# Performance work log

Hardware: AMD Instinct MI355X
Metric: run time of the kernel (lower is better)

Reference implementation:

```python
import jax, jax.numpy as jnp
import numpy as np

N = 16384      # total points
B = 8          # point clouds in batch
PER = N // B   # points per cloud (batch ids sorted in blocks)
M = 4096       # sampled centers (ratio 0.25, strided sampler -> batch-aligned)
K = 64         # max_num_neighbors
R = 0.25       # ball-query radius
C_IN = 128
HID = 256
C_OUT = 256


def setup_inputs() -> dict:
    key = jax.random.key(0)
    k1, k2, k3, k4, k5 = jax.random.split(key, 5)
    x = jax.random.normal(k1, (N, C_IN), dtype=jnp.float32)
    pos = jax.random.uniform(k2, (N, 3), dtype=jnp.float32)  # unit cube
    batch = jnp.repeat(jnp.arange(B, dtype=jnp.int32), PER)  # sorted block batch ids
    lframes = jax.random.normal(k3, (N, 3, 3), dtype=jnp.float32)
    W1 = jax.random.normal(k4, (2 * C_IN + 3, HID), dtype=jnp.float32) * 0.05
    b1 = jnp.zeros((HID,), dtype=jnp.float32)
    W2 = jax.random.normal(k5, (HID, C_OUT), dtype=jnp.float32) * 0.05
    b2 = jnp.zeros((C_OUT,), dtype=jnp.float32)
    return {"x": x, "pos": pos, "batch": batch, "lframes": lframes,
            "W1": W1, "b1": b1, "W2": W2, "b2": b2}


def _ball_query(pos, batch, idx):
    """radius(pos, pos[idx], R, batch, batch[idx], max_num_neighbors=K).
    Returns fixed-size neighbor indices [M, K] + validity mask [M, K]."""
    pos_c = pos[idx]                                  # [M, 3]
    # squared distances via gemm trick (avoid [M, N, 3] broadcast)
    d2 = ((pos_c ** 2).sum(-1)[:, None]
          + (pos ** 2).sum(-1)[None, :]
          - 2.0 * pos_c @ pos.T)                      # [M, N]
    valid = (d2 <= R * R) & (batch[idx][:, None] == batch[None, :])
    score = jnp.where(valid, -d2, -jnp.inf)
    vals, nbr = jax.lax.top_k(score, K)               # K nearest within ball
    return nbr, jnp.isfinite(vals)


def reference(x, pos, batch, lframes, W1, b1, W2, b2):
    # center sampler: strided subsample (batch-aligned since batch is block-sorted)
    idx = jnp.arange(0, N, N // M)                    # [M]
    nbr, vmask = _ball_query(pos, batch, idx)         # [M, K]

    pos_dst = pos[idx]                                # [M, 3]
    x_dst = x[idx]                                    # [M, C_IN]
    lframes_dst = lframes[idx]                        # [M, 3, 3]

    # EdgeConv: per-edge message MLP([x_src, x_dst, lframe_dst @ (pos_src - pos_dst)])
    rel = pos[nbr] - pos_dst[:, None, :]              # [M, K, 3]
    rel_loc = jnp.einsum('mij,mkj->mki', lframes_dst, rel)  # rotate into dst frame
    feats = jnp.concatenate([
        x[nbr],                                        # [M, K, C_IN]
        jnp.broadcast_to(x_dst[:, None, :], (M, K, C_IN)),
        rel_loc,
    ], axis=-1)                                        # [M, K, 2*C_IN+3]

    h = jax.nn.relu(feats @ W1 + b1)                   # [M, K, HID]
    msg = h @ W2 + b2                                  # [M, K, C_OUT]

    # masked max aggregation over valid neighbors
    msg = jnp.where(vmask[..., None], msg, -jnp.inf)
    out = msg.max(axis=1)                              # [M, C_OUT]
    out = jnp.where(jnp.isfinite(out), out, 0.0)
    return out, pos_dst, batch[idx], lframes_dst
```

## Files before the change

kernel.cpp:

```cpp
#include <hip/hip_runtime.h>
#include <hip/hip_bf16.h>

#define N_PTS 16384
#define PER   2048
#define M_CTR 4096
#define KNB   64
#define C_IN  128
#define HID   256
#define C_OUT 256

typedef unsigned short u16;
typedef unsigned int u32;
typedef __attribute__((ext_vector_type(8))) short s8v;
typedef __attribute__((ext_vector_type(4))) float f4v;
typedef __attribute__((ext_vector_type(4))) unsigned int u4v;

static __device__ __forceinline__ u16 f2bf(float f) {
    union { float f; unsigned int i; } v; v.f = f;
    unsigned int r = v.i + 0x7FFFu + ((v.i >> 16) & 1u);
    return (u16)(r >> 16);
}

__global__ __launch_bounds__(256) void ballq_kernel(
        const float* __restrict__ pos, int* __restrict__ nbr, int* __restrict__ cnt,
        const float* __restrict__ W1, const float* __restrict__ W2,
        u16* __restrict__ W1aT, u16* __restrict__ W1bT, u16* __restrict__ W2T) {
    __shared__ float cd2[1024];
    __shared__ int   cidx[1024];
    __shared__ int   s_n;
    int m = blockIdx.x, tid = threadIdx.x;

    if (m < 256) {
        int gid = m * 256 + tid;
        int cc = gid >> 8, k = gid & 255;
        W2T[gid] = f2bf(W2[k * 256 + cc]);
        if (gid < 32768) {
            int c1 = gid >> 7, k1 = gid & 127;
            W1aT[gid] = f2bf(W1[k1 * 256 + c1]);
            W1bT[gid] = f2bf(W1[(k1 + 128) * 256 + c1]);
        }
    }

    int c = m * 4;
    int base = (m >> 9) << 11;
    int ln = tid & 63;
    if (tid == 0) s_n = 0;
    __syncthreads();
    float cx = pos[c * 3 + 0], cy = pos[c * 3 + 1], cz = pos[c * 3 + 2];
    float A = __fadd_rn(__fadd_rn(__fmul_rn(cx, cx), __fmul_rn(cy, cy)), __fmul_rn(cz, cz));
    float c2x = __fmul_rn(2.0f, cx);
    float c2y = __fmul_rn(2.0f, cy);
    float c2z = __fmul_rn(2.0f, cz);
    for (int s = 0; s < 8; ++s) {
        int j = base + tid + (s << 8);
        float px = pos[j * 3 + 0], py = pos[j * 3 + 1], pz = pos[j * 3 + 2];
        float B = __fadd_rn(__fadd_rn(__fmul_rn(px, px), __fmul_rn(py, py)), __fmul_rn(pz, pz));
        float C = __fmaf_rn(c2z, pz, __fmaf_rn(c2y, py, __fmul_rn(c2x, px)));
        float d2 = __fsub_rn(__fadd_rn(A, B), C);
        bool hit = (d2 <= 0.0625f);
        unsigned long long mk = __ballot(hit);
        int nb = __popcll(mk & ((1ull << ln) - 1ull));
        int tot = __popcll(mk);
        int bidx = 0;
        if (ln == 0 && tot) bidx = atomicAdd(&s_n, tot);
        bidx = __shfl(bidx, 0, 64);
        if (hit) {
            int a = bidx + nb;
            if (a < 1024) { cd2[a] = d2; cidx[a] = j; }
        }
    }
    __syncthreads();
    int V = s_n < 1024 ? s_n : 1024;
    if (V <= KNB) {
        if (tid < KNB) nbr[m * KNB + tid] = (tid < V) ? cidx[tid] : c;
        if (tid == 0) cnt[m] = V;
    } else {
        for (int e = tid; e < V; e += 256) {
            float de = cd2[e]; int ie = cidx[e];
            int rank = 0;
            for (int q = 0; q < V; ++q) {
                float dq = cd2[q];
                rank += (dq < de) || (dq == de && cidx[q] < ie);
            }
            if (rank < KNB) nbr[m * KNB + rank] = cidx[e];
        }
        if (tid == 0) cnt[m] = KNB;
    }
}

__global__ __launch_bounds__(256) void gemm_xw_kernel(
        const float* __restrict__ x, const u16* __restrict__ W1aT, const u16* __restrict__ W1bT,
        const float* __restrict__ b1, u16* __restrict__ u_out, float* __restrict__ v_out) {
    __shared__ u16 x_lds[64 * 136];
    int blk = blockIdx.x, tid = threadIdx.x;
    int mode = blk >= 256 ? 1 : 0;
    int bb = mode ? blk - 256 : blk;
    const u16* WT = mode ? W1bT : W1aT;
    {
        int r = tid >> 2, q = tid & 3;
        int xrow = bb * 64 + r;
        if (mode) xrow *= 4;
        const float* xp = x + xrow * C_IN + q * 32;
        u16* dst = x_lds + r * 136 + q * 32;
        for (int i = 0; i < 8; ++i) {
            f4v f = *(const f4v*)(xp + i * 4);
            dst[i * 4 + 0] = f2bf(f[0]);
            dst[i * 4 + 1] = f2bf(f[1]);
            dst[i * 4 + 2] = f2bf(f[2]);
            dst[i * 4 + 3] = f2bf(f[3]);
        }
    }
    __syncthreads();
    int lane = tid & 63, w = tid >> 6;
    int quad = lane >> 4, l16 = lane & 15;
    int cb = w * 64;
    f4v acc[4][4] = {};
    for (int k0 = 0; k0 < 128; k0 += 32) {
        s8v a[4], b[4];
        for (int rt = 0; rt < 4; ++rt)
            a[rt] = *(const s8v*)&x_lds[(rt * 16 + l16) * 136 + k0 + quad * 8];
        for (int ct = 0; ct < 4; ++ct)
            b[ct] = *(const s8v*)(WT + (cb + ct * 16 + l16) * 128 + k0 + quad * 8);
        for (int rt = 0; rt < 4; ++rt)
            for (int ct = 0; ct < 4; ++ct)
                acc[rt][ct] = __builtin_amdgcn_mfma_f32_16x16x32_bf16(a[rt], b[ct], acc[rt][ct], 0, 0, 0);
    }
    for (int rt = 0; rt < 4; ++rt)
        for (int ct = 0; ct < 4; ++ct)
            for (int g = 0; g < 4; ++g) {
                int row = rt * 16 + quad * 4 + g;
                int col = cb + ct * 16 + l16;
                float val = acc[rt][ct][g];
                int orow = bb * 64 + row;
                if (mode == 0) u_out[orow * 256 + col] = f2bf(val);
                else           v_out[orow * 256 + col] = val + b1[col];
            }
}

__global__ __launch_bounds__(512, 2) void edge_kernel(
        const u16* __restrict__ u, const float* __restrict__ v,
        const u16* __restrict__ W2T, const float* __restrict__ W1,
        const float* __restrict__ b2, const float* __restrict__ pos,
        const float* __restrict__ lframes, const int* __restrict__ batch,
        const int* __restrict__ nbrg, const int* __restrict__ cnt,
        float* __restrict__ out0, float* __restrict__ out_pos,
        float* __restrict__ out_batch, float* __restrict__ out_lf) {
    __shared__ u16   h_lds[2][128 * 264];
    __shared__ float v_lds[2][2][256];
    __shared__ float w1c_lds[768];
    __shared__ f4v   relc_lds[2][2][64];
    __shared__ u16   nbr_lds[2][2][64];

    int blk = blockIdx.x, tid = threadIdx.x;
    int m0 = ((blk & 7) << 9) | ((blk >> 3) << 3);

    int lane = tid & 63, w = tid >> 6;
    int quad = lane >> 4, l16 = lane & 15;
    int cb = (w & 3) * 64;
    int rbase = (w >> 2) * 64;
    int gsel = w >> 2;

    s8v bfrag[6][4];
    #pragma unroll
    for (int k0 = 0; k0 < 6; ++k0)
        #pragma unroll
        for (int ct = 0; ct < 4; ++ct)
            bfrag[k0][ct] = *(const s8v*)(W2T + (cb + ct * 16 + l16) * 256 + k0 * 32 + quad * 8);

    for (int i = tid; i < 768; i += 512) w1c_lds[i] = W1[65536 + i];
    if (tid < 128) {
        int g = tid >> 6, t = tid & 63;
        int mm = m0 + g, cc = mm * 4;
        int j = nbrg[mm * KNB + t];
        nbr_lds[0][g][t] = (u16)j;
        float rx = pos[j * 3 + 0] - pos[cc * 3 + 0];
        float ry = pos[j * 3 + 1] - pos[cc * 3 + 1];
        float rz = pos[j * 3 + 2] - pos[cc * 3 + 2];
        const float* lf = lframes + cc * 9;
        f4v r;
        r[0] = lf[0] * rx + lf[1] * ry + lf[2] * rz;
        r[1] = lf[3] * rx + lf[4] * ry + lf[5] * rz;
        r[2] = lf[6] * rx + lf[7] * ry + lf[8] * rz;
        r[3] = 0.0f;
        relc_lds[0][g][t] = r;
    }
    v_lds[0][tid >> 8][tid & 255] = v[(m0 + (tid >> 8)) * 256 + (tid & 255)];
    if (tid >= 256 && tid < 384) {
        int g = (tid - 256) >> 4, t = tid & 15;
        int mm = m0 + g, cc = mm * 4;
        if (t < 3)            out_pos[mm * 3 + t] = pos[cc * 3 + t];
        else if (t == 3)      out_batch[mm] = (float)batch[cc];
        else if (t < 13)      out_lf[mm * 9 + (t - 4)] = lframes[cc * 9 + (t - 4)];
    }

    int co = (tid & 31) * 8;
    int rs = tid >> 5;
    int cv_cur = cnt[m0 + gsel];
    __syncthreads();

    int cv_next = 0;
    for (int p = 0; p < 4; ++p) {
        int pb = p & 1;
        #pragma unroll
        for (int g = 0; g < 2; ++g) {
            f4v vq0 = *(const f4v*)&v_lds[pb][g][co];
            f4v vq1 = *(const f4v*)&v_lds[pb][g][co + 4];
            f4v wa0 = *(const f4v*)&w1c_lds[co],       wa1 = *(const f4v*)&w1c_lds[co + 4];
            f4v wb0 = *(const f4v*)&w1c_lds[256 + co], wb1 = *(const f4v*)&w1c_lds[256 + co + 4];
            f4v wc0 = *(const f4v*)&w1c_lds[512 + co], wc1 = *(const f4v*)&w1c_lds[512 + co + 4];
            #pragma unroll
            for (int i2 = 0; i2 < 4; ++i2) {
                int rl = rs + i2 * 16;
                int row = g * 64 + rl;
                int j = (int)nbr_lds[pb][g][rl];
                u4v uu = *(const u4v*)(u + j * 256 + co);
                f4v r = relc_lds[pb][g][rl];
                float p8[8];
                #pragma unroll
                for (int e = 0; e < 8; ++e) {
                    u32 bits = (e & 1) ? (uu[e >> 1] & 0xFFFF0000u) : (uu[e >> 1] << 16);
                    float va = (e < 4) ? vq0[e] : vq1[e - 4];
                    float a0 = (e < 4) ? wa0[e] : wa1[e - 4];
                    float b0 = (e < 4) ? wb0[e] : wb1[e - 4];
                    float c0 = (e < 4) ? wc0[e] : wc1[e - 4];
                    float pre = fmaf(r[0], a0, fmaf(r[1], b0, fmaf(r[2], c0,
                                  va + __uint_as_float(bits))));
                    p8[e] = fmaxf(pre, 0.0f);
                }
                u4v pk;
                #pragma unroll
                for (int d = 0; d < 4; ++d)
                    pk[d] = __builtin_amdgcn_perm(__float_as_uint(p8[2 * d + 1]),
                                                  __float_as_uint(p8[2 * d]), 0x07060302u);
                *(u4v*)&h_lds[pb][row * 264 + co] = pk;
            }
        }
        if (p < 3) {
            int nb = pb ^ 1;
            int mbase = m0 + (p + 1) * 2;
            cv_next = cnt[mbase + gsel];
            if (tid < 128) {
                int g = tid >> 6, t = tid & 63;
                int mm = mbase + g, cc = mm * 4;
                int j = nbrg[mm * KNB + t];
                nbr_lds[nb][g][t] = (u16)j;
                float rx = pos[j * 3 + 0] - pos[cc * 3 + 0];
                float ry = pos[j * 3 + 1] - pos[cc * 3 + 1];
                float rz = pos[j * 3 + 2] - pos[cc * 3 + 2];
                const float* lf = lframes + cc * 9;
                f4v r;
                r[0] = lf[0] * rx + lf[1] * ry + lf[2] * rz;
                r[1] = lf[3] * rx + lf[4] * ry + lf[5] * rz;
                r[2] = lf[6] * rx + lf[7] * ry + lf[8] * rz;
                r[3] = 0.0f;
                relc_lds[nb][g][t] = r;
            }
            v_lds[nb][tid >> 8][tid & 255] = v[(mbase + (tid >> 8)) * 256 + (tid & 255)];
        }
        __syncthreads();

        s8v bs[2][4];
        #pragma unroll
        for (int kk = 0; kk < 2; ++kk)
            #pragma unroll
            for (int ct = 0; ct < 4; ++ct)
                bs[kk][ct] = *(const s8v*)(W2T + (cb + ct * 16 + l16) * 256 + (6 + kk) * 32 + quad * 8);
        f4v acc[4][4] = {};
        #pragma unroll
        for (int k0 = 0; k0 < 6; ++k0) {
            s8v a[4];
            #pragma unroll
            for (int rt = 0; rt < 4; ++rt)
                a[rt] = *(const s8v*)&h_lds[pb][(rbase + rt * 16 + l16) * 264 + k0 * 32 + quad * 8];
            #pragma unroll
            for (int rt = 0; rt < 4; ++rt)
                #pragma unroll
                for (int ct = 0; ct < 4; ++ct)
                    acc[rt][ct] = __builtin_amdgcn_mfma_f32_16x16x32_bf16(a[rt], bfrag[k0][ct], acc[rt][ct], 0, 0, 0);
        }
        #pragma unroll
        for (int kk = 0; kk < 2; ++kk) {
            int k0 = 6 + kk;
            s8v a[4];
            #pragma unroll
            for (int rt = 0; rt < 4; ++rt)
                a[rt] = *(const s8v*)&h_lds[pb][(rbase + rt * 16 + l16) * 264 + k0 * 32 + quad * 8];
            #pragma unroll
            for (int rt = 0; rt < 4; ++rt)
                #pragma unroll
                for (int ct = 0; ct < 4; ++ct)
                    acc[rt][ct] = __builtin_amdgcn_mfma_f32_16x16x32_bf16(a[rt], bs[kk][ct], acc[rt][ct], 0, 0, 0);
        }
        int mout = m0 + p * 2 + gsel;
        #pragma unroll
        for (int ct = 0; ct < 4; ++ct) {
            float mx = -__builtin_inff();
            #pragma unroll
            for (int rt = 0; rt < 4; ++rt)
                #pragma unroll
                for (int g = 0; g < 4; ++g) {
                    int row = rt * 16 + quad * 4 + g;
                    float val = acc[rt][ct][g];
                    if (row < cv_cur) mx = fmaxf(mx, val);
                }
            mx = fmaxf(mx, __shfl_xor(mx, 16, 64));
            mx = fmaxf(mx, __shfl_xor(mx, 32, 64));
            if (lane < 16)
                out0[mout * 256 + cb + ct * 16 + l16] = mx + b2[cb + ct * 16 + l16];
        }
        cv_cur = cv_next;
    }
}

extern "C" void kernel_launch(void* const* d_in, const int* in_sizes, int n_in,
                              void* d_out, int out_size, void* d_ws, size_t ws_size,
                              hipStream_t stream) {
    const float* x       = (const float*)d_in[0];
    const float* pos     = (const float*)d_in[1];
    const int*   batch   = (const int*)d_in[2];
    const float* lframes = (const float*)d_in[3];
    const float* W1      = (const float*)d_in[4];
    const float* b1      = (const float*)d_in[5];
    const float* W2      = (const float*)d_in[6];
    const float* b2      = (const float*)d_in[7];

    float* out       = (float*)d_out;
    float* out_pos   = out + M_CTR * 256;
    float* out_batch = out_pos + M_CTR * 3;
    float* out_lf    = out_batch + M_CTR;

    char* ws = (char*)d_ws;
    u16*   u_ws = (u16*)(ws);
    float* v_ws = (float*)(ws + 8388608);
    u16*   W1aT = (u16*)(ws + 12582912);
    u16*   W1bT = (u16*)(ws + 12648448);
    u16*   W2T  = (u16*)(ws + 12713984);
    int*   nbr  = (int*)(ws + 12845056);
    int*   cntp = (int*)(ws + 13893632);

    hipLaunchKernelGGL(ballq_kernel, dim3(M_CTR), dim3(256), 0, stream,
                       pos, nbr, cntp, W1, W2, W1aT, W1bT, W2T);
    hipLaunchKernelGGL(gemm_xw_kernel, dim3(320), dim3(256), 0, stream,
                       x, W1aT, W1bT, b1, u_ws, v_ws);
    hipLaunchKernelGGL(edge_kernel, dim3(512), dim3(512), 0, stream,
                       u_ws, v_ws, W2T, W1, b2, pos, lframes, batch, nbr, cntp,
                       out, out_pos, out_batch, out_lf);
}
```

Before: 172.0 us.

## Preload all per-center metadata upfront and prefetch neighbor rows into registers

All four center-pair stages of neighbor indices, rotated relative positions and v rows are now loaded into LDS once in the prologue, with the v rows copied as vector loads. Per-stage LDS double-buffer refills are removed. The gathered bf16 u rows for the next stage are issued into registers right after the barrier, so their latency overlaps the MFMA work of the current stage. This costs extra registers for the prefetched rows and a little more LDS, which may hurt occupancy at 512 threads with two blocks per CU.

```diff
diff --git a/kernel.cpp b/kernel.cpp
--- a/kernel.cpp
+++ b/kernel.cpp
@@ -146,10 +146,10 @@
         float* __restrict__ out0, float* __restrict__ out_pos,
         float* __restrict__ out_batch, float* __restrict__ out_lf) {
     __shared__ u16   h_lds[2][128 * 264];
-    __shared__ float v_lds[2][2][256];
+    __shared__ float v_lds[4][2][256];
     __shared__ float w1c_lds[768];
-    __shared__ f4v   relc_lds[2][2][64];
-    __shared__ u16   nbr_lds[2][2][64];
+    __shared__ f4v   relc_lds[4][2][64];
+    __shared__ u16   nbr_lds[4][2][64];
 
     int blk = blockIdx.x, tid = threadIdx.x;
     int m0 = ((blk & 7) << 9) | ((blk >> 3) << 3);
@@ -168,11 +168,11 @@
             bfrag[k0][ct] = *(const s8v*)(W2T + (cb + ct * 16 + l16) * 256 + k0 * 32 + quad * 8);
 
     for (int i = tid; i < 768; i += 512) w1c_lds[i] = W1[65536 + i];
-    if (tid < 128) {
-        int g = tid >> 6, t = tid & 63;
-        int mm = m0 + g, cc = mm * 4;
+    {
+        int pr = tid >> 7, g = (tid >> 6) & 1, t = tid & 63;
+        int mm = m0 + pr * 2 + g, cc = mm * 4;
         int j = nbrg[mm * KNB + t];
-        nbr_lds[0][g][t] = (u16)j;
+        nbr_lds[pr][g][t] = (u16)j;
         float rx = pos[j * 3 + 0] - pos[cc * 3 + 0];
         float ry = pos[j * 3 + 1] - pos[cc * 3 + 1];
         float rz = pos[j * 3 + 2] - pos[cc * 3 + 2];
@@ -182,9 +182,9 @@
         r[1] = lf[3] * rx + lf[4] * ry + lf[5] * rz;
         r[2] = lf[6] * rx + lf[7] * ry + lf[8] * rz;
         r[3] = 0.0f;
-        relc_lds[0][g][t] = r;
-    }
-    v_lds[0][tid >> 8][tid & 255] = v[(m0 + (tid >> 8)) * 256 + (tid & 255)];
+        relc_lds[pr][g][t] = r;
+    }
+    ((f4v*)v_lds)[tid] = *(const f4v*)(v + m0 * 256 + tid * 4);
     if (tid >= 256 && tid < 384) {
         int g = (tid - 256) >> 4, t = tid & 15;
         int mm = m0 + g, cc = mm * 4;
@@ -195,16 +195,25 @@
 
     int co = (tid & 31) * 8;
     int rs = tid >> 5;
-    int cv_cur = cnt[m0 + gsel];
+
+    u4v ug[8];
+    #pragma unroll
+    for (int g = 0; g < 2; ++g)
+        #pragma unroll
+        for (int i2 = 0; i2 < 4; ++i2) {
+            int rl = rs + i2 * 16;
+            int j = nbrg[(m0 + g) * KNB + rl];
+            ug[g * 4 + i2] = *(const u4v*)(u + j * 256 + co);
+        }
     __syncthreads();
 
-    int cv_next = 0;
     for (int p = 0; p < 4; ++p) {
         int pb = p & 1;
+        int cvp = cnt[m0 + p * 2 + gsel];
         #pragma unroll
         for (int g = 0; g < 2; ++g) {
-            f4v vq0 = *(const f4v*)&v_lds[pb][g][co];
-            f4v vq1 = *(const f4v*)&v_lds[pb][g][co + 4];
+            f4v vq0 = *(const f4v*)&v_lds[p][g][co];
+            f4v vq1 = *(const f4v*)&v_lds[p][g][co + 4];
             f4v wa0 = *(const f4v*)&w1c_lds[co],       wa1 = *(const f4v*)&w1c_lds[co + 4];
             f4v wb0 = *(const f4v*)&w1c_lds[256 + co], wb1 = *(const f4v*)&w1c_lds[256 + co + 4];
             f4v wc0 = *(const f4v*)&w1c_lds[512 + co], wc1 = *(const f4v*)&w1c_lds[512 + co + 4];
@@ -212,9 +221,8 @@
             for (int i2 = 0; i2 < 4; ++i2) {
                 int rl = rs + i2 * 16;
                 int row = g * 64 + rl;
-                int j = (int)nbr_lds[pb][g][rl];
-                u4v uu = *(const u4v*)(u + j * 256 + co);
-                f4v r = relc_lds[pb][g][rl];
+                u4v uu = ug[g * 4 + i2];
+                f4v r = relc_lds[p][g][rl];
                 float p8[8];
                 #pragma unroll
                 for (int e = 0; e < 8; ++e) {
@@ -235,29 +243,18 @@
                 *(u4v*)&h_lds[pb][row * 264 + co] = pk;
             }
         }
+        __syncthreads();
+
         if (p < 3) {
-            int nb = pb ^ 1;
-            int mbase = m0 + (p + 1) * 2;
-            cv_next = cnt[mbase + gsel];
-            if (tid < 128) {
-                int g = tid >> 6, t = tid & 63;
-                int mm = mbase + g, cc = mm * 4;
-                int j = nbrg[mm * KNB + t];
-                nbr_lds[nb][g][t] = (u16)j;
-                float rx = pos[j * 3 + 0] - pos[cc * 3 + 0];
-                float ry = pos[j * 3 + 1] - pos[cc * 3 + 1];
-                float rz = pos[j * 3 + 2] - pos[cc * 3 + 2];
-                const float* lf = lframes + cc * 9;
-                f4v r;
-                r[0] = lf[0] * rx + lf[1] * ry + lf[2] * rz;
-                r[1] = lf[3] * rx + lf[4] * ry + lf[5] * rz;
-                r[2] = lf[6] * rx + lf[7] * ry + lf[8] * rz;
-                r[3] = 0.0f;
-                relc_lds[nb][g][t] = r;
-            }
-            v_lds[nb][tid >> 8][tid & 255] = v[(mbase + (tid >> 8)) * 256 + (tid & 255)];
-        }
-        __syncthreads();
+            #pragma unroll
+            for (int g = 0; g < 2; ++g)
+                #pragma unroll
+                for (int i2 = 0; i2 < 4; ++i2) {
+                    int rl = rs + i2 * 16;
+                    int j = (int)nbr_lds[p + 1][g][rl];
+                    ug[g * 4 + i2] = *(const u4v*)(u + j * 256 + co);
+                }
+        }
 
         s8v bs[2][4];
         #pragma unroll
@@ -301,14 +298,13 @@
                 for (int g = 0; g < 4; ++g) {
                     int row = rt * 16 + quad * 4 + g;
                     float val = acc[rt][ct][g];
-                    if (row < cv_cur) mx = fmaxf(mx, val);
+                    if (row < cvp) mx = fmaxf(mx, val);
                 }
             mx = fmaxf(mx, __shfl_xor(mx, 16, 64));
             mx = fmaxf(mx, __shfl_xor(mx, 32, 64));
             if (lane < 16)
                 out0[mout * 256 + cb + ct * 16 + l16] = mx + b2[cb + ct * 16 + l16];
         }
-        cv_cur = cv_next;
     }
 }
 
```

Measured after the change: 179.6 us. 1.04x slower.
